# Optimization experiments

Measured on AMD Instinct MI355X. Metric: run time of the kernel, lower is better.

Reference implementation:

```python
import jax, jax.numpy as jnp
import numpy as np

B, L, D, H, V = 4, 2048, 512, 8, 50257
NCAND, K, MAXM, NL, DFF = 64, 5, 10, 2, 4 * 512
HD = D // H


def _ln(x, g, b, eps=1e-5):
    m = jnp.mean(x, -1, keepdims=True)
    v = jnp.mean((x - m) ** 2, -1, keepdims=True)
    return (x - m) * jax.lax.rsqrt(v + eps) * g + b


def _mha(x, in_w, in_b, out_w, out_b):
    Bx, Lx, Dx = x.shape
    qkv = x @ in_w.T + in_b                      # [B,L,3D]
    q, k, v = jnp.split(qkv, 3, axis=-1)
    heads = lambda t: t.reshape(Bx, Lx, H, HD).transpose(0, 2, 1, 3)  # [B,H,L,hd]
    q, k, v = heads(q), heads(k), heads(v)
    s = jnp.einsum('bhqd,bhkd->bhqk', q, k) * np.float32(1.0 / np.sqrt(HD))
    a = jax.nn.softmax(s, axis=-1)
    o = jnp.einsum('bhqk,bhkd->bhqd', a, v).transpose(0, 2, 1, 3).reshape(Bx, Lx, Dx)
    return o @ out_w.T + out_b


def _encoder(x, p):
    # torch TransformerEncoderLayer default: post-LN, ReLU, dropout off (eval)
    for i in range(NL):
        x = _ln(x + _mha(x, p['attn_in_w'][i], p['attn_in_b'][i], p['attn_out_w'][i], p['attn_out_b'][i]), p['ln1_g'][i], p['ln1_b'][i])
        h = jax.nn.relu(x @ p['ffn_w1'][i].T + p['ffn_b1'][i]) @ p['ffn_w2'][i].T + p['ffn_b2'][i]
        x = _ln(x + h, p['ln2_g'][i], p['ln2_b'][i])
    return x


def _forward(token_ids, candidate_embeds, p):
    x = p['tok_emb'][token_ids] + p['pos_emb'][jnp.arange(L)][None]
    hidden = _encoder(x, p)                                  # [B,L,D]
    start_logits = hidden @ p['start_w'] + p['start_b']      # [B,L]
    end_logits = hidden @ p['end_w'] + p['end_b']
    s_idx = jax.lax.top_k(start_logits, K)[1]                # [B,K]
    e_idx = jax.lax.top_k(end_logits, K)[1]
    valid = (e_idx >= s_idx) & ((e_idx - s_idx) < MAXM)      # span validity mask
    h_s = jnp.take_along_axis(hidden, s_idx[..., None], axis=1)  # [B,K,D]
    h_e = jnp.take_along_axis(hidden, e_idx[..., None], axis=1)
    feat = jnp.concatenate([h_s, h_e, h_s * h_e], axis=-1)   # [B,K,3D]
    span = jax.nn.relu(feat @ p['span_w1'].T + p['span_b1']) @ p['span_w2'].T + p['span_b2']
    # compact valid spans to the front (ragged-to-padded), pad rest with zeros
    order = jnp.argsort((~valid).astype(jnp.int32), axis=1)  # stable: valid first
    span = jnp.take_along_axis(span, order[..., None], axis=1)
    vs = jnp.take_along_axis(valid, order, axis=1)
    span = span * vs[..., None].astype(span.dtype)           # [B,K,D]
    mp = span @ p['mention_w'].T + p['mention_b']
    cp = candidate_embeds @ p['entity_w'].T + p['entity_b']
    scores = jnp.einsum('bmd,bmcd->bmc', mp, cp)             # [B,K,NCAND]
    return span, start_logits, end_logits, hidden, scores


PARAM_KEYS = ['tok_emb', 'pos_emb', 'attn_in_w', 'attn_in_b', 'attn_out_w', 'attn_out_b',
              'ln1_g', 'ln1_b', 'ffn_w1', 'ffn_b1', 'ffn_w2', 'ffn_b2', 'ln2_g', 'ln2_b',
              'start_w', 'start_b', 'end_w', 'end_b', 'span_w1', 'span_b1', 'span_w2', 'span_b2',
              'mention_w', 'mention_b', 'entity_w', 'entity_b']


def setup_inputs() -> dict:
    key = jax.random.key(0)
    ks = iter(jax.random.split(key, 32))
    n = lambda shape, s=0.02: jax.random.normal(next(ks), shape, jnp.float32) * s
    return {
        'token_ids': jax.random.randint(next(ks), (B, L), 0, V),
        'candidate_embeds': jax.random.normal(next(ks), (B, K, NCAND, D), jnp.float32),
        'tok_emb': n((V, D)), 'pos_emb': n((L, D)),
        'attn_in_w': n((NL, 3 * D, D)), 'attn_in_b': n((NL, 3 * D)),
        'attn_out_w': n((NL, D, D)), 'attn_out_b': n((NL, D)),
        'ln1_g': jnp.ones((NL, D)), 'ln1_b': jnp.zeros((NL, D)),
        'ffn_w1': n((NL, DFF, D)), 'ffn_b1': n((NL, DFF)),
        'ffn_w2': n((NL, D, DFF)), 'ffn_b2': n((NL, D)),
        'ln2_g': jnp.ones((NL, D)), 'ln2_b': jnp.zeros((NL, D)),
        'start_w': n((D,)), 'start_b': jnp.zeros(()),
        'end_w': n((D,)), 'end_b': jnp.zeros(()),
        'span_w1': n((D, 3 * D)), 'span_b1': jnp.zeros((D,)),
        'span_w2': n((D, D)), 'span_b2': jnp.zeros((D,)),
        'mention_w': n((D, D)), 'mention_b': jnp.zeros((D,)),
        'entity_w': n((D, D)), 'entity_b': jnp.zeros((D,)),
    }


def reference(token_ids, candidate_embeds, tok_emb, pos_emb, attn_in_w, attn_in_b, attn_out_w, attn_out_b,
              ln1_g, ln1_b, ffn_w1, ffn_b1, ffn_w2, ffn_b2, ln2_g, ln2_b,
              start_w, start_b, end_w, end_b, span_w1, span_b1, span_w2, span_b2,
              mention_w, mention_b, entity_w, entity_b):
    loc = locals()
    p = {k: loc[k] for k in PARAM_KEYS}
    return _forward(token_ids, candidate_embeds, p)
```

## Files before the change

### kernel.cpp

```cpp
#include <hip/hip_runtime.h>
#include <hip/hip_bf16.h>
#include <cstddef>

#define BQ 4
#define LQ 2048
#define DQ 512
#define HQ 8
#define HDQ 64
#define KQ 5
#define MAXMQ 10

typedef __attribute__((ext_vector_type(8))) __bf16 bf16x8;
typedef __attribute__((ext_vector_type(4))) __bf16 bf16x4;
typedef __attribute__((ext_vector_type(4))) float f32x4;

__device__ inline void gload_lds16(const void* g, void* l) {
  __builtin_amdgcn_global_load_lds(
      (const __attribute__((address_space(1))) unsigned*)g,
      (__attribute__((address_space(3))) unsigned*)l, 16, 0, 0);
}

__device__ inline unsigned pack_bf16(float a, float b) {
  unsigned short ua = __builtin_bit_cast(unsigned short, (__bf16)a);
  unsigned short ub = __builtin_bit_cast(unsigned short, (__bf16)b);
  return (unsigned)ua | ((unsigned)ub << 16);
}

__device__ inline unsigned pack2(__bf16 a, __bf16 b) {
  return (unsigned)__builtin_bit_cast(unsigned short, a) |
         ((unsigned)__builtin_bit_cast(unsigned short, b) << 16);
}

__device__ inline float bf_lo(unsigned u) {
  return (float)__builtin_bit_cast(__bf16, (unsigned short)(u & 0xffff));
}
__device__ inline float bf_hi(unsigned u) {
  return (float)__builtin_bit_cast(__bf16, (unsigned short)(u >> 16));
}

__global__ __launch_bounds__(256) void prep_kernel(
    const float* __restrict__ s0, const float* __restrict__ s1,
    const float* __restrict__ s2, const float* __restrict__ s3,
    __bf16* __restrict__ d0, __bf16* __restrict__ d1,
    __bf16* __restrict__ d2, __bf16* __restrict__ d3,
    const float* __restrict__ ew_in, float* __restrict__ ew_out,
    const int* __restrict__ tok, const float* __restrict__ te,
    const float* __restrict__ pe, __bf16* __restrict__ xb) {
  __shared__ float t[32][33];
  const int bid = blockIdx.x;
  if (bid < 3072) {
    size_t g = ((size_t)bid * 256 + threadIdx.x) * 8;
    const float* src; __bf16* dst; size_t e;
    if (g < 1572864)      { src = s0; dst = d0; e = g; }
    else if (g < 2097152) { src = s1; dst = d1; e = g - 1572864; }
    else if (g < 4194304) { src = s2; dst = d2; e = g - 2097152; }
    else                  { src = s3; dst = d3; e = g - 4194304; }
    float4 a = *(const float4*)(src + e);
    float4 b = *(const float4*)(src + e + 4);
    bf16x8 v;
    v[0] = (__bf16)a.x; v[1] = (__bf16)a.y; v[2] = (__bf16)a.z; v[3] = (__bf16)a.w;
    v[4] = (__bf16)b.x; v[5] = (__bf16)b.y; v[6] = (__bf16)b.z; v[7] = (__bf16)b.w;
    *(bf16x8*)(dst + e) = v;
  } else if (bid < 3328) {
    int blk = bid - 3072;
    int bx = blk & 15, by = blk >> 4;
    int cx = threadIdx.x & 31, ry = threadIdx.x >> 5;
    #pragma unroll
    for (int i = 0; i < 4; ++i)
      t[ry + i * 8][cx] = ew_in[(size_t)(by * 32 + ry + i * 8) * 512 + bx * 32 + cx];
    __syncthreads();
    #pragma unroll
    for (int i = 0; i < 4; ++i)
      ew_out[(size_t)(bx * 32 + ry + i * 8) * 512 + by * 32 + cx] = t[cx][ry + i * 8];
  } else {
    int row = bid - 3328;
    int l = row & (LQ - 1);
    int tk = tok[row];
    int d = 2 * threadIdx.x;
    float2 tv = *(const float2*)&te[(size_t)tk * DQ + d];
    float2 pv = *(const float2*)&pe[(size_t)l * DQ + d];
    *(unsigned*)&xb[(size_t)row * DQ + d] = pack_bf16(tv.x + pv.x, tv.y + pv.y);
  }
}

template<bool RELU>
__global__ __launch_bounds__(256) void bgemm_kernel(
    const __bf16* __restrict__ A, const __bf16* __restrict__ W,
    const float* __restrict__ bias, __bf16* __restrict__ Cb,
    int M, int N, int K) {
  __shared__ __bf16 As[2][128][32];
  __shared__ __bf16 Bs[2][128][32];
  const int tid = threadIdx.x;
  const int w = tid >> 6, lane = tid & 63;
  const int lr = lane & 15, lg = lane >> 4;
  const int wr = w >> 1, wc = w & 1;
  const int m0 = blockIdx.y * 128, n0 = blockIdx.x * 128;

  f32x4 acc[4][4];
  #pragma unroll
  for (int m = 0; m < 4; ++m)
    #pragma unroll
    for (int n = 0; n < 4; ++n) acc[m][n] = f32x4{0.f, 0.f, 0.f, 0.f};

  const int srow = w * 32 + (lane >> 2);
  const int scol = (lane & 3) * 8;
  const __bf16* Ag = A + (size_t)(m0 + srow) * K + scol;
  const __bf16* Bg = W + (size_t)(n0 + srow) * K + scol;

  const int NT = K / 32;

  auto stage = [&](int t, int buf) {
    const int k1 = t * 32;
    gload_lds16(Ag + k1, &As[buf][w * 32][0]);
    gload_lds16(Ag + 16 * K + k1, &As[buf][w * 32 + 16][0]);
    gload_lds16(Bg + k1, &Bs[buf][w * 32][0]);
    gload_lds16(Bg + 16 * K + k1, &Bs[buf][w * 32 + 16][0]);
  };

  auto step = [&](int t, int cur) {
    __syncthreads();
    if (t + 1 < NT) stage(t + 1, cur ^ 1);
    bf16x8 af[4], bfr[4];
    #pragma unroll
    for (int m = 0; m < 4; ++m) af[m] = *(bf16x8*)&As[cur][wr * 64 + m * 16 + lr][lg * 8];
    #pragma unroll
    for (int n = 0; n < 4; ++n) bfr[n] = *(bf16x8*)&Bs[cur][wc * 64 + n * 16 + lr][lg * 8];
    __builtin_amdgcn_s_setprio(1);
    #pragma unroll
    for (int m = 0; m < 4; ++m)
      #pragma unroll
      for (int n = 0; n < 4; ++n)
        acc[m][n] = __builtin_amdgcn_mfma_f32_16x16x32_bf16(af[m], bfr[n], acc[m][n], 0, 0, 0);
    __builtin_amdgcn_s_setprio(0);
  };

  stage(0, 0);
  for (int t = 0; t < NT; t += 2) { step(t, 0); step(t + 1, 1); }

  const int crow = m0 + wr * 64 + lg * 4;
  const int ccol = n0 + wc * 64 + lr;
  #pragma unroll
  for (int n = 0; n < 4; ++n) {
    int gc = ccol + n * 16;
    float bn = bias[gc];
    #pragma unroll
    for (int m = 0; m < 4; ++m) {
      #pragma unroll
      for (int reg = 0; reg < 4; ++reg) {
        int gr = crow + m * 16 + reg;
        float v = acc[m][n][reg] + bn;
        if (RELU) v = fmaxf(v, 0.f);
        Cb[(size_t)gr * N + gc] = (__bf16)v;
      }
    }
  }
}

__global__ __launch_bounds__(256) void bgemm_sk_kernel(
    const __bf16* __restrict__ A, const __bf16* __restrict__ W,
    float* __restrict__ P, int M, int N, int K) {
  __shared__ __bf16 As[2][128][32];
  __shared__ __bf16 Bs[2][128][32];
  const int tid = threadIdx.x;
  const int w = tid >> 6, lane = tid & 63;
  const int lr = lane & 15, lg = lane >> 4;
  const int wr = w >> 1, wc = w & 1;
  const int m0 = blockIdx.y * 128, n0 = blockIdx.x * 128;
  const int ks = blockIdx.z;
  const int kh = K / 2;

  f32x4 acc[4][4];
  #pragma unroll
  for (int m = 0; m < 4; ++m)
    #pragma unroll
    for (int n = 0; n < 4; ++n) acc[m][n] = f32x4{0.f, 0.f, 0.f, 0.f};

  const int srow = w * 32 + (lane >> 2);
  const int scol = (lane & 3) * 8;
  const __bf16* Ag = A + (size_t)(m0 + srow) * K + ks * kh + scol;
  const __bf16* Bg = W + (size_t)(n0 + srow) * K + ks * kh + scol;

  const int NT = kh / 32;

  auto stage = [&](int t, int buf) {
    const int k1 = t * 32;
    gload_lds16(Ag + k1, &As[buf][w * 32][0]);
    gload_lds16(Ag + 16 * K + k1, &As[buf][w * 32 + 16][0]);
    gload_lds16(Bg + k1, &Bs[buf][w * 32][0]);
    gload_lds16(Bg + 16 * K + k1, &Bs[buf][w * 32 + 16][0]);
  };

  auto step = [&](int t, int cur) {
    __syncthreads();
    if (t + 1 < NT) stage(t + 1, cur ^ 1);
    bf16x8 af[4], bfr[4];
    #pragma unroll
    for (int m = 0; m < 4; ++m) af[m] = *(bf16x8*)&As[cur][wr * 64 + m * 16 + lr][lg * 8];
    #pragma unroll
    for (int n = 0; n < 4; ++n) bfr[n] = *(bf16x8*)&Bs[cur][wc * 64 + n * 16 + lr][lg * 8];
    __builtin_amdgcn_s_setprio(1);
    #pragma unroll
    for (int m = 0; m < 4; ++m)
      #pragma unroll
      for (int n = 0; n < 4; ++n)
        acc[m][n] = __builtin_amdgcn_mfma_f32_16x16x32_bf16(af[m], bfr[n], acc[m][n], 0, 0, 0);
    __builtin_amdgcn_s_setprio(0);
  };

  stage(0, 0);
  for (int t = 0; t < NT; t += 2) { step(t, 0); step(t + 1, 1); }

  float* Pk = P + (size_t)ks * M * N;
  const int crow = m0 + wr * 64 + lg * 4;
  const int ccol = n0 + wc * 64 + lr;
  #pragma unroll
  for (int n = 0; n < 4; ++n) {
    int gc = ccol + n * 16;
    #pragma unroll
    for (int m = 0; m < 4; ++m)
      #pragma unroll
      for (int reg = 0; reg < 4; ++reg)
        Pk[(size_t)(crow + m * 16 + reg) * N + gc] = acc[m][n][reg];
  }
}

template<bool FIN>
__global__ __launch_bounds__(256) void lnc_kernel(
    const float* __restrict__ P, const float* __restrict__ bias,
    __bf16* __restrict__ Xb, const float* __restrict__ g,
    const float* __restrict__ bb, float* __restrict__ xf,
    const float* __restrict__ sw, const float* __restrict__ sb,
    const float* __restrict__ ew, const float* __restrict__ eb,
    float* __restrict__ osl, float* __restrict__ oel) {
  int row = blockIdx.x;
  int tid = threadIdx.x;
  int d = 2 * tid;
  float2 p0 = *(const float2*)&P[(size_t)row * DQ + d];
  float2 p1 = *(const float2*)&P[(size_t)(BQ * LQ) * DQ + (size_t)row * DQ + d];
  float2 bi = *(const float2*)&bias[d];
  unsigned ur = *(const unsigned*)&Xb[(size_t)row * DQ + d];
  float v0 = p0.x + p1.x + bi.x + bf_lo(ur);
  float v1 = p0.y + p1.y + bi.y + bf_hi(ur);
  float s = v0 + v1, ss = v0 * v0 + v1 * v1;
  #pragma unroll
  for (int off = 32; off; off >>= 1) { s += __shfl_xor(s, off); ss += __shfl_xor(ss, off); }
  __shared__ float rs[4], rss[4];
  int w = tid >> 6;
  if ((tid & 63) == 0) { rs[w] = s; rss[w] = ss; }
  __syncthreads();
  s = rs[0] + rs[1] + rs[2] + rs[3];
  ss = rss[0] + rss[1] + rss[2] + rss[3];
  float mean = s * (1.f / 512.f);
  float var = ss * (1.f / 512.f) - mean * mean;
  float r = rsqrtf(var + 1e-5f);
  float2 gg = *(const float2*)&g[d];
  float2 bv = *(const float2*)&bb[d];
  float o0 = (v0 - mean) * r * gg.x + bv.x;
  float o1 = (v1 - mean) * r * gg.y + bv.y;
  *(unsigned*)&Xb[(size_t)row * DQ + d] = pack_bf16(o0, o1);
  if (FIN) {
    float2 of; of.x = o0; of.y = o1;
    *(float2*)&xf[(size_t)row * DQ + d] = of;
    float2 swv = *(const float2*)&sw[d];
    float2 ewv = *(const float2*)&ew[d];
    float a = o0 * swv.x + o1 * swv.y;
    float b2 = o0 * ewv.x + o1 * ewv.y;
    #pragma unroll
    for (int off = 32; off; off >>= 1) { a += __shfl_xor(a, off); b2 += __shfl_xor(b2, off); }
    __shared__ float ra[4], rb[4];
    if ((tid & 63) == 0) { ra[w] = a; rb[w] = b2; }
    __syncthreads();
    if (tid == 0) {
      osl[row] = ra[0] + ra[1] + ra[2] + ra[3] + sb[0];
      oel[row] = rb[0] + rb[1] + rb[2] + rb[3] + eb[0];
    }
  }
}

template<int MR, bool RELU, bool MASK>
__global__ __launch_bounds__(256) void tinygemm_kernel(
    const float* __restrict__ A, const float* __restrict__ W,
    const float* __restrict__ bias, const int* __restrict__ vs,
    float* __restrict__ C, int N, int K) {
  int n = blockIdx.x * 4 + (threadIdx.x >> 6);
  int lane = threadIdx.x & 63;
  if (n >= N) return;
  const float* wr = W + (size_t)n * K;
  float acc[MR];
  #pragma unroll
  for (int m = 0; m < MR; ++m) acc[m] = 0.f;
  for (int k = lane; k < K; k += 64) {
    float wv = wr[k];
    #pragma unroll
    for (int m = 0; m < MR; ++m)
      acc[m] += A[(size_t)m * K + k] * wv;
  }
  #pragma unroll
  for (int m = 0; m < MR; ++m) {
    #pragma unroll
    for (int off = 32; off; off >>= 1) acc[m] += __shfl_xor(acc[m], off);
  }
  if (lane == 0) {
    float bn = bias ? bias[n] : 0.f;
    #pragma unroll
    for (int m = 0; m < MR; ++m) {
      float v = acc[m] + bn;
      if (RELU) v = fmaxf(v, 0.f);
      if (MASK) v *= (float)vs[m];
      C[(size_t)m * N + n] = v;
    }
  }
}

__global__ __launch_bounds__(512) void attn_mfma_kernel(const __bf16* __restrict__ qkv,
                                                        __bf16* __restrict__ ob) {
  __shared__ __bf16 Ks[2][4096];
  __shared__ __bf16 Vt[2][64][72];
  __shared__ __bf16 Ps[8][1024];

  const int tid = threadIdx.x;
  const int wave = tid >> 6;
  const int lane = tid & 63;
  const int lr = lane & 15;
  const int lg = lane >> 4;

  const int bid = blockIdx.x;
  const int swz = (bid & 7) * 64 + (bid >> 3);
  const int bh = swz >> 4;
  const int qb = swz & 15;
  const int b = bh >> 3, h = bh & 7;
  const int q0 = qb * 128 + wave * 16;

  const __bf16* base = qkv + (size_t)b * LQ * 1536;

  bf16x8 aq[2];
  {
    const __bf16* qp = base + (size_t)(q0 + lr) * 1536 + h * 64 + lg * 8;
    aq[0] = *(const bf16x8*)qp;
    aq[1] = *(const bf16x8*)(qp + 32);
  }

  const int krow = tid >> 3;
  const int kdc = (tid & 7) ^ (krow & 7);
  const __bf16* gK = base + (size_t)krow * 1536 + 512 + h * 64 + kdc * 8;

  const int pr2 = tid >> 4;
  const int dq = tid & 15;
  const int vd0 = dq * 4;
  const __bf16* gV = base + (size_t)(2 * pr2) * 1536 + 1024 + h * 64 + vd0;
  const int pc2 = 2 * (pr2 & 3) + 8 * ((pr2 >> 2) ^ (dq >> 1));

  const int STEP = 64 * 1536;

  float lsum = 0.f;
  f32x4 o_acc[4];
  #pragma unroll
  for (int df = 0; df < 4; ++df) o_acc[df] = f32x4{0.f, 0.f, 0.f, 0.f};

  const float KE = 0.125f * 1.44269504f;

  gload_lds16(gK, &Ks[0][64 * wave * 8]);
  {
    bf16x4 v0 = *(const bf16x4*)gV;
    bf16x4 v1 = *(const bf16x4*)(gV + 1536);
    #pragma unroll
    for (int i = 0; i < 4; ++i)
      *(unsigned*)&Vt[0][vd0 + i][pc2] = pack2(v0[i], v1[i]);
  }
  gK += STEP; gV += STEP;

  auto tile = [&](int cur, bool more) {
    __syncthreads();
    bf16x4 nv0, nv1;
    if (more) {
      gload_lds16(gK, &Ks[cur ^ 1][64 * wave * 8]);
      nv0 = *(const bf16x4*)gV;
      nv1 = *(const bf16x4*)(gV + 1536);
      gK += STEP; gV += STEP;
    }

    f32x4 s[4];
    __builtin_amdgcn_s_setprio(1);
    #pragma unroll
    for (int f = 0; f < 4; ++f) {
      f32x4 acc = f32x4{0.f, 0.f, 0.f, 0.f};
      #pragma unroll
      for (int c = 0; c < 2; ++c) {
        bf16x8 ak = *(bf16x8*)&Ks[cur][(f * 16 + lr) * 64 + (((4 * c + lg) ^ (lr & 7)) << 3)];
        acc = __builtin_amdgcn_mfma_f32_16x16x32_bf16(ak, aq[c], acc, 0, 0, 0);
      }
      s[f] = acc;
    }
    __builtin_amdgcn_s_setprio(0);

    float rs = 0.f;
    #pragma unroll
    for (int f = 0; f < 4; ++f)
      #pragma unroll
      for (int r = 0; r < 4; ++r) {
        float p = exp2f(s[f][r] * KE);
        s[f][r] = p;
        rs += p;
      }
    rs += __shfl_xor(rs, 16);
    rs += __shfl_xor(rs, 32);
    lsum += rs;

    #pragma unroll
    for (int f = 0; f < 4; ++f) {
      uint2 pv;
      pv.x = pack_bf16(s[f][0], s[f][1]);
      pv.y = pack_bf16(s[f][2], s[f][3]);
      int chunk = 2 * f + (lg >> 1);
      int eoff = ((chunk ^ (lr & 7)) << 3) + ((lg & 1) << 2);
      *(uint2*)&Ps[wave][lr * 64 + eoff] = pv;
    }

    #pragma unroll
    for (int kc = 0; kc < 2; ++kc) {
      bf16x8 bp = *(bf16x8*)&Ps[wave][lr * 64 + (((4 * kc + lg) ^ (lr & 7)) << 3)];
      __builtin_amdgcn_s_setprio(1);
      #pragma unroll
      for (int df = 0; df < 4; ++df) {
        int vrow = df * 16 + lr;
        int pb = (((4 * kc + lg) ^ ((vrow >> 3) & 7)) << 3);
        bf16x8 av = *(bf16x8*)&Vt[cur][vrow][pb];
        o_acc[df] = __builtin_amdgcn_mfma_f32_16x16x32_bf16(av, bp, o_acc[df], 0, 0, 0);
      }
      __builtin_amdgcn_s_setprio(0);
    }

    if (more) {
      #pragma unroll
      for (int i = 0; i < 4; ++i)
        *(unsigned*)&Vt[cur ^ 1][vd0 + i][pc2] = pack2(nv0[i], nv1[i]);
    }
  };

  for (int kt = 0; kt < LQ / 64; kt += 2) {
    tile(0, true);
    tile(1, kt + 1 != LQ / 64 - 1);
  }

  float inv = 1.f / lsum;
  __bf16* orow = ob + ((size_t)(b * LQ) + q0 + lr) * DQ + h * 64 + lg * 4;
  #pragma unroll
  for (int df = 0; df < 4; ++df) {
    uint2 ov;
    ov.x = pack_bf16(o_acc[df][0] * inv, o_acc[df][1] * inv);
    ov.y = pack_bf16(o_acc[df][2] * inv, o_acc[df][3] * inv);
    *(uint2*)(orow + df * 16) = ov;
  }
}

__global__ void topkvo_kernel(const float* __restrict__ slog, const float* __restrict__ elog,
                              int* __restrict__ sidx, int* __restrict__ eidx,
                              int* __restrict__ order, int* __restrict__ vs) {
  int b = blockIdx.x;
  int which = threadIdx.x >> 6;
  int lane = threadIdx.x & 63;
  const float* lg = (which ? elog : slog) + (size_t)b * LQ;
  int* outp = (which ? eidx : sidx) + b * KQ;
  __shared__ int sel[2][KQ];
  int ch[KQ];
  for (int k = 0; k < KQ; ++k) {
    float bv = -1e38f; int bi = 1 << 30;
    for (int i = lane; i < LQ; i += 64) {
      bool skip = false;
      for (int t = 0; t < k; ++t) if (ch[t] == i) skip = true;
      float v = lg[i];
      if (!skip && (v > bv || (v == bv && i < bi))) { bv = v; bi = i; }
    }
    #pragma unroll
    for (int off = 32; off; off >>= 1) {
      float ov = __shfl_xor(bv, off); int oi = __shfl_xor(bi, off);
      if (ov > bv || (ov == bv && oi < bi)) { bv = ov; bi = oi; }
    }
    ch[k] = bi;
    if (lane == 0) { outp[k] = bi; sel[which][k] = bi; }
  }
  __syncthreads();
  if (threadIdx.x == 0) {
    int val[KQ];
    for (int k = 0; k < KQ; ++k) {
      int s = sel[0][k], e = sel[1][k];
      val[k] = (e >= s && (e - s) < MAXMQ) ? 1 : 0;
    }
    int j = 0;
    for (int k = 0; k < KQ; ++k) if (val[k])  { order[b * KQ + j] = k; vs[b * KQ + j] = 1; ++j; }
    for (int k = 0; k < KQ; ++k) if (!val[k]) { order[b * KQ + j] = k; vs[b * KQ + j] = 0; ++j; }
  }
}

__global__ __launch_bounds__(256) void feat_kernel(const float* __restrict__ hidden,
    const int* __restrict__ sidx, const int* __restrict__ eidx,
    const int* __restrict__ order, float* __restrict__ feat) {
  int row = blockIdx.x;
  int b = row / KQ;
  int k = order[row];
  int si = sidx[b * KQ + k], ei = eidx[b * KQ + k];
  const float* hs = hidden + ((size_t)(b * LQ + si)) * DQ;
  const float* he = hidden + ((size_t)(b * LQ + ei)) * DQ;
  float* fr = feat + (size_t)row * (3 * DQ);
  for (int d = threadIdx.x; d < DQ; d += 256) {
    float a = hs[d], c = he[d];
    fr[d] = a; fr[DQ + d] = c; fr[2 * DQ + d] = a * c;
  }
}

__global__ __launch_bounds__(256) void scores_kernel(const float* __restrict__ cand,
    const float* __restrict__ mp, const float* __restrict__ u, const float* __restrict__ ebias,
    float* __restrict__ oscores) {
  int gw = blockIdx.x * 4 + (threadIdx.x >> 6);
  int lane = threadIdx.x & 63;
  int bj = gw >> 6;
  const float* ce = cand + (size_t)gw * DQ;
  const float* ur = u + (size_t)bj * DQ;
  const float* mr = mp + (size_t)bj * DQ;
  float s = 0.f;
  #pragma unroll
  for (int i = 0; i < 8; ++i) {
    int e = lane + i * 64;
    s += ce[e] * ur[e] + mr[e] * ebias[e];
  }
  #pragma unroll
  for (int off = 32; off; off >>= 1) s += __shfl_xor(s, off);
  if (lane == 0) oscores[gw] = s;
}

extern "C" void kernel_launch(void* const* d_in, const int* in_sizes, int n_in,
                              void* d_out, int out_size, void* d_ws, size_t ws_size,
                              hipStream_t stream) {
  const int*   token_ids = (const int*)d_in[0];
  const float* cand    = (const float*)d_in[1];
  const float* tok_emb = (const float*)d_in[2];
  const float* pos_emb = (const float*)d_in[3];
  const float* ain_w   = (const float*)d_in[4];
  const float* ain_b   = (const float*)d_in[5];
  const float* aout_w  = (const float*)d_in[6];
  const float* aout_b  = (const float*)d_in[7];
  const float* ln1g    = (const float*)d_in[8];
  const float* ln1b    = (const float*)d_in[9];
  const float* fw1     = (const float*)d_in[10];
  const float* fb1     = (const float*)d_in[11];
  const float* fw2     = (const float*)d_in[12];
  const float* fb2     = (const float*)d_in[13];
  const float* ln2g    = (const float*)d_in[14];
  const float* ln2b    = (const float*)d_in[15];
  const float* sw      = (const float*)d_in[16];
  const float* sb      = (const float*)d_in[17];
  const float* ew      = (const float*)d_in[18];
  const float* eb      = (const float*)d_in[19];
  const float* sp_w1   = (const float*)d_in[20];
  const float* sp_b1   = (const float*)d_in[21];
  const float* sp_w2   = (const float*)d_in[22];
  const float* sp_b2   = (const float*)d_in[23];
  const float* m_w     = (const float*)d_in[24];
  const float* m_b     = (const float*)d_in[25];
  const float* e_w     = (const float*)d_in[26];
  const float* e_b     = (const float*)d_in[27];

  const int M = BQ * LQ;
  float* out = (float*)d_out;
  float* out_span   = out;
  float* out_sl     = out + 10240;
  float* out_el     = out + 18432;
  float* out_hidden = out + 26624;
  float* out_scores = out + 4220928;

  float* ws  = (float*)d_ws;
  __bf16* BIGb = (__bf16*)ws;
  __bf16* Xb   = (__bf16*)(ws + 8388608);
  __bf16* Ob   = (__bf16*)(ws + 10485760);
  float*  Pbuf = ws + 12582912;
  __bf16* ain_wb  = (__bf16*)(ws + 20971520);
  __bf16* aout_wb = (__bf16*)(ws + 21757952);
  __bf16* fw1b    = (__bf16*)(ws + 22020096);
  __bf16* fw2b    = (__bf16*)(ws + 23068672);
  float* e_wT     = ws + 24117248;
  int*   SIDX  = (int*)(ws + 24379392);
  int*   EIDX  = SIDX + 20;
  int*   ORDER = EIDX + 20;
  int*   VS    = ORDER + 20;
  float* FEAT    = ws + 24379520;
  float* SPANH   = FEAT + 30720;
  float* MP      = SPANH + 10240;
  float* U       = MP + 10240;

  prep_kernel<<<11520, 256, 0, stream>>>(ain_w, aout_w, fw1, fw2,
                                         ain_wb, aout_wb, fw1b, fw2b,
                                         e_w, e_wT, token_ids, tok_emb, pos_emb, Xb);

  for (int l = 0; l < 2; ++l) {
    bgemm_kernel<false><<<dim3(12, 64), 256, 0, stream>>>(
        Xb, ain_wb + (size_t)l * 1536 * 512, ain_b + l * 1536, BIGb, M, 1536, 512);
    attn_mfma_kernel<<<512, 512, 0, stream>>>(BIGb, Ob);
    bgemm_sk_kernel<<<dim3(4, 64, 2), 256, 0, stream>>>(
        Ob, aout_wb + (size_t)l * 512 * 512, Pbuf, M, 512, 512);
    lnc_kernel<false><<<M, 256, 0, stream>>>(
        Pbuf, aout_b + l * 512, Xb, ln1g + l * 512, ln1b + l * 512,
        nullptr, nullptr, nullptr, nullptr, nullptr, nullptr, nullptr);
    bgemm_kernel<true><<<dim3(16, 64), 256, 0, stream>>>(
        Xb, fw1b + (size_t)l * 2048 * 512, fb1 + l * 2048, BIGb, M, 2048, 512);
    bgemm_sk_kernel<<<dim3(4, 64, 2), 256, 0, stream>>>(
        BIGb, fw2b + (size_t)l * 512 * 2048, Pbuf, M, 512, 2048);
    if (l == 0)
      lnc_kernel<false><<<M, 256, 0, stream>>>(
          Pbuf, fb2, Xb, ln2g, ln2b,
          nullptr, nullptr, nullptr, nullptr, nullptr, nullptr, nullptr);
    else
      lnc_kernel<true><<<M, 256, 0, stream>>>(
          Pbuf, fb2 + 512, Xb, ln2g + 512, ln2b + 512,
          out_hidden, sw, sb, ew, eb, out_sl, out_el);
  }

  topkvo_kernel<<<4, 128, 0, stream>>>(out_sl, out_el, SIDX, EIDX, ORDER, VS);
  feat_kernel<<<20, 256, 0, stream>>>(out_hidden, SIDX, EIDX, ORDER, FEAT);
  tinygemm_kernel<20, true, false><<<128, 256, 0, stream>>>(
      FEAT, sp_w1, sp_b1, nullptr, SPANH, 512, 1536);
  tinygemm_kernel<20, false, true><<<128, 256, 0, stream>>>(
      SPANH, sp_w2, sp_b2, VS, out_span, 512, 512);
  tinygemm_kernel<20, false, false><<<128, 256, 0, stream>>>(
      out_span, m_w, m_b, nullptr, MP, 512, 512);
  tinygemm_kernel<20, false, false><<<128, 256, 0, stream>>>(
      MP, e_wT, nullptr, nullptr, U, 512, 512);
  scores_kernel<<<320, 256, 0, stream>>>(cand, MP, U, e_b, out_scores);
}
```

Baseline: 467.1 us.

## Switch attention to 32x32x16 MFMA with 4 waves of 32 query rows

The attention kernel now uses 32x32x16 bf16 MFMA tiles instead of 16x16x32, so each wave covers 32 query rows and the block drops from 8 waves to 4 while keeping 128 queries per block. K and V staging, the P layout in LDS and the output write are rearranged to match the larger fragment shape. Each wave now loads half as many K/V fragments per query, which cuts LDS traffic and instruction count per FLOP. In exchange there are fewer waves per block to hide latency and more accumulator registers per lane, which may lower occupancy.

```diff
diff --git a/kernel.cpp b/kernel.cpp
--- a/kernel.cpp
+++ b/kernel.cpp
@@ -13,6 +13,7 @@
 typedef __attribute__((ext_vector_type(8))) __bf16 bf16x8;
 typedef __attribute__((ext_vector_type(4))) __bf16 bf16x4;
 typedef __attribute__((ext_vector_type(4))) float f32x4;
+typedef __attribute__((ext_vector_type(16))) float f32x16;
 
 __device__ inline void gload_lds16(const void* g, void* l) {
   __builtin_amdgcn_global_load_lds(
@@ -312,128 +313,122 @@
   }
 }
 
-__global__ __launch_bounds__(512) void attn_mfma_kernel(const __bf16* __restrict__ qkv,
+__global__ __launch_bounds__(256) void attn_mfma_kernel(const __bf16* __restrict__ qkv,
                                                         __bf16* __restrict__ ob) {
   __shared__ __bf16 Ks[2][4096];
   __shared__ __bf16 Vt[2][64][72];
-  __shared__ __bf16 Ps[8][1024];
+  __shared__ __bf16 Ps[4][2048];
 
   const int tid = threadIdx.x;
   const int wave = tid >> 6;
   const int lane = tid & 63;
-  const int lr = lane & 15;
-  const int lg = lane >> 4;
+  const int l31 = lane & 31;
+  const int hi = lane >> 5;
 
   const int bid = blockIdx.x;
   const int swz = (bid & 7) * 64 + (bid >> 3);
   const int bh = swz >> 4;
   const int qb = swz & 15;
   const int b = bh >> 3, h = bh & 7;
-  const int q0 = qb * 128 + wave * 16;
+  const int q0 = qb * 128 + wave * 32;
 
   const __bf16* base = qkv + (size_t)b * LQ * 1536;
 
-  bf16x8 aq[2];
+  bf16x8 bq[4];
   {
-    const __bf16* qp = base + (size_t)(q0 + lr) * 1536 + h * 64 + lg * 8;
-    aq[0] = *(const bf16x8*)qp;
-    aq[1] = *(const bf16x8*)(qp + 32);
+    const __bf16* qp = base + (size_t)(q0 + l31) * 1536 + h * 64 + 8 * hi;
+    bq[0] = *(const bf16x8*)qp;
+    bq[1] = *(const bf16x8*)(qp + 16);
+    bq[2] = *(const bf16x8*)(qp + 32);
+    bq[3] = *(const bf16x8*)(qp + 48);
   }
 
   const int krow = tid >> 3;
   const int kdc = (tid & 7) ^ (krow & 7);
-  const __bf16* gK = base + (size_t)krow * 1536 + 512 + h * 64 + kdc * 8;
-
-  const int pr2 = tid >> 4;
-  const int dq = tid & 15;
-  const int vd0 = dq * 4;
-  const __bf16* gV = base + (size_t)(2 * pr2) * 1536 + 1024 + h * 64 + vd0;
-  const int pc2 = 2 * (pr2 & 3) + 8 * ((pr2 >> 2) ^ (dq >> 1));
+  const __bf16* gK0 = base + (size_t)krow * 1536 + 512 + h * 64 + kdc * 8;
+  const __bf16* gK1 = gK0 + 32 * 1536;
+
+  const int pr = tid >> 3, vdc = tid & 7;
+  const __bf16* gV = base + (size_t)(2 * pr) * 1536 + 1024 + h * 64 + vdc * 8;
+  const int pc2 = 2 * (pr & 3) + 8 * ((pr >> 2) ^ vdc);
 
   const int STEP = 64 * 1536;
 
   float lsum = 0.f;
-  f32x4 o_acc[4];
-  #pragma unroll
-  for (int df = 0; df < 4; ++df) o_acc[df] = f32x4{0.f, 0.f, 0.f, 0.f};
+  f32x16 oacc[2];
+  #pragma unroll
+  for (int r = 0; r < 16; ++r) { oacc[0][r] = 0.f; oacc[1][r] = 0.f; }
 
   const float KE = 0.125f * 1.44269504f;
 
-  gload_lds16(gK, &Ks[0][64 * wave * 8]);
+  gload_lds16(gK0, &Ks[0][wave * 512]);
+  gload_lds16(gK1, &Ks[0][2048 + wave * 512]);
   {
-    bf16x4 v0 = *(const bf16x4*)gV;
-    bf16x4 v1 = *(const bf16x4*)(gV + 1536);
-    #pragma unroll
-    for (int i = 0; i < 4; ++i)
-      *(unsigned*)&Vt[0][vd0 + i][pc2] = pack2(v0[i], v1[i]);
-  }
-  gK += STEP; gV += STEP;
+    bf16x8 v0 = *(const bf16x8*)gV;
+    bf16x8 v1 = *(const bf16x8*)(gV + 1536);
+    #pragma unroll
+    for (int i = 0; i < 8; ++i)
+      *(unsigned*)&Vt[0][vdc * 8 + i][pc2] = pack2(v0[i], v1[i]);
+  }
+  gK0 += STEP; gK1 += STEP; gV += STEP;
 
   auto tile = [&](int cur, bool more) {
     __syncthreads();
-    bf16x4 nv0, nv1;
+    bf16x8 nv0, nv1;
     if (more) {
-      gload_lds16(gK, &Ks[cur ^ 1][64 * wave * 8]);
-      nv0 = *(const bf16x4*)gV;
-      nv1 = *(const bf16x4*)(gV + 1536);
-      gK += STEP; gV += STEP;
-    }
-
-    f32x4 s[4];
-    __builtin_amdgcn_s_setprio(1);
-    #pragma unroll
-    for (int f = 0; f < 4; ++f) {
-      f32x4 acc = f32x4{0.f, 0.f, 0.f, 0.f};
-      #pragma unroll
-      for (int c = 0; c < 2; ++c) {
-        bf16x8 ak = *(bf16x8*)&Ks[cur][(f * 16 + lr) * 64 + (((4 * c + lg) ^ (lr & 7)) << 3)];
-        acc = __builtin_amdgcn_mfma_f32_16x16x32_bf16(ak, aq[c], acc, 0, 0, 0);
+      gload_lds16(gK0, &Ks[cur ^ 1][wave * 512]);
+      gload_lds16(gK1, &Ks[cur ^ 1][2048 + wave * 512]);
+      nv0 = *(const bf16x8*)gV;
+      nv1 = *(const bf16x8*)(gV + 1536);
+      gK0 += STEP; gK1 += STEP; gV += STEP;
+    }
+
+    float rs = 0.f;
+    #pragma unroll
+    for (int pos = 0; pos < 2; ++pos) {
+      f32x16 acc;
+      #pragma unroll
+      for (int r = 0; r < 16; ++r) acc[r] = 0.f;
+      __builtin_amdgcn_s_setprio(1);
+      #pragma unroll
+      for (int ks = 0; ks < 4; ++ks) {
+        bf16x8 ak = *(bf16x8*)&Ks[cur][(pos * 32 + l31) * 64 +
+                                       (((2 * ks + hi) ^ (l31 & 7)) << 3)];
+        acc = __builtin_amdgcn_mfma_f32_32x32x16_bf16(ak, bq[ks], acc, 0, 0, 0);
       }
-      s[f] = acc;
-    }
-    __builtin_amdgcn_s_setprio(0);
-
-    float rs = 0.f;
-    #pragma unroll
-    for (int f = 0; f < 4; ++f)
-      #pragma unroll
-      for (int r = 0; r < 4; ++r) {
-        float p = exp2f(s[f][r] * KE);
-        s[f][r] = p;
-        rs += p;
+      __builtin_amdgcn_s_setprio(0);
+      float p[16];
+      #pragma unroll
+      for (int r = 0; r < 16; ++r) { p[r] = exp2f(acc[r] * KE); rs += p[r]; }
+      #pragma unroll
+      for (int g = 0; g < 4; ++g) {
+        uint2 pv;
+        pv.x = pack_bf16(p[4 * g], p[4 * g + 1]);
+        pv.y = pack_bf16(p[4 * g + 2], p[4 * g + 3]);
+        int c = 4 * pos + g;
+        *(uint2*)&Ps[wave][l31 * 64 + ((c ^ (l31 & 7)) << 3) + (hi << 2)] = pv;
       }
-    rs += __shfl_xor(rs, 16);
+    }
     rs += __shfl_xor(rs, 32);
     lsum += rs;
 
     #pragma unroll
-    for (int f = 0; f < 4; ++f) {
-      uint2 pv;
-      pv.x = pack_bf16(s[f][0], s[f][1]);
-      pv.y = pack_bf16(s[f][2], s[f][3]);
-      int chunk = 2 * f + (lg >> 1);
-      int eoff = ((chunk ^ (lr & 7)) << 3) + ((lg & 1) << 2);
-      *(uint2*)&Ps[wave][lr * 64 + eoff] = pv;
-    }
-
-    #pragma unroll
-    for (int kc = 0; kc < 2; ++kc) {
-      bf16x8 bp = *(bf16x8*)&Ps[wave][lr * 64 + (((4 * kc + lg) ^ (lr & 7)) << 3)];
+    for (int ks2 = 0; ks2 < 4; ++ks2) {
+      bf16x8 bp = *(bf16x8*)&Ps[wave][l31 * 64 + (((2 * ks2 + hi) ^ (l31 & 7)) << 3)];
       __builtin_amdgcn_s_setprio(1);
       #pragma unroll
-      for (int df = 0; df < 4; ++df) {
-        int vrow = df * 16 + lr;
-        int pb = (((4 * kc + lg) ^ ((vrow >> 3) & 7)) << 3);
-        bf16x8 av = *(bf16x8*)&Vt[cur][vrow][pb];
-        o_acc[df] = __builtin_amdgcn_mfma_f32_16x16x32_bf16(av, bp, o_acc[df], 0, 0, 0);
+      for (int pd = 0; pd < 2; ++pd) {
+        int d = pd * 32 + l31;
+        bf16x8 av = *(bf16x8*)&Vt[cur][d][(((2 * ks2 + hi) ^ ((d >> 3) & 7)) << 3)];
+        oacc[pd] = __builtin_amdgcn_mfma_f32_32x32x16_bf16(av, bp, oacc[pd], 0, 0, 0);
       }
       __builtin_amdgcn_s_setprio(0);
     }
 
     if (more) {
       #pragma unroll
-      for (int i = 0; i < 4; ++i)
-        *(unsigned*)&Vt[cur ^ 1][vd0 + i][pc2] = pack2(nv0[i], nv1[i]);
+      for (int i = 0; i < 8; ++i)
+        *(unsigned*)&Vt[cur ^ 1][vdc * 8 + i][pc2] = pack2(nv0[i], nv1[i]);
     }
   };
 
@@ -443,13 +438,16 @@
   }
 
   float inv = 1.f / lsum;
-  __bf16* orow = ob + ((size_t)(b * LQ) + q0 + lr) * DQ + h * 64 + lg * 4;
-  #pragma unroll
-  for (int df = 0; df < 4; ++df) {
-    uint2 ov;
-    ov.x = pack_bf16(o_acc[df][0] * inv, o_acc[df][1] * inv);
-    ov.y = pack_bf16(o_acc[df][2] * inv, o_acc[df][3] * inv);
-    *(uint2*)(orow + df * 16) = ov;
+  __bf16* orow = ob + ((size_t)(b * LQ) + q0 + l31) * DQ + h * 64 + 4 * hi;
+  #pragma unroll
+  for (int pd = 0; pd < 2; ++pd) {
+    #pragma unroll
+    for (int g = 0; g < 4; ++g) {
+      uint2 ov;
+      ov.x = pack_bf16(oacc[pd][4 * g] * inv, oacc[pd][4 * g + 1] * inv);
+      ov.y = pack_bf16(oacc[pd][4 * g + 2] * inv, oacc[pd][4 * g + 3] * inv);
+      *(uint2*)(orow + pd * 32 + g * 8) = ov;
+    }
   }
 }
 
@@ -594,7 +592,7 @@
   for (int l = 0; l < 2; ++l) {
     bgemm_kernel<false><<<dim3(12, 64), 256, 0, stream>>>(
         Xb, ain_wb + (size_t)l * 1536 * 512, ain_b + l * 1536, BIGb, M, 1536, 512);
-    attn_mfma_kernel<<<512, 512, 0, stream>>>(BIGb, Ob);
+    attn_mfma_kernel<<<512, 256, 0, stream>>>(BIGb, Ob);
     bgemm_sk_kernel<<<dim3(4, 64, 2), 256, 0, stream>>>(
         Ob, aout_wb + (size_t)l * 512 * 512, Pbuf, M, 512, 512);
     lnc_kernel<false><<<M, 256, 0, stream>>>(
```

After: 478.6 us. +2.5%, slower.
